# Optimization experiments

Hardware: AMD Instinct MI355X
Metric: run time of the kernel (lower is better)

## Reference

```python
import jax, jax.numpy as jnp
import numpy as np

N = 16384          # number of points (single graph, batch all-zero)
K = 20             # kNN neighbors (DynamicEdgeConv k=20), includes self like torch_cluster.knn
FEATURE_DIM = 128


def setup_inputs() -> dict:
    key = jax.random.key(0)
    ks = jax.random.split(key, 6)
    def lin(k, fan_in, fan_out):
        return (jax.random.normal(k, (fan_in, fan_out), dtype=jnp.float32)
                / np.float32(np.sqrt(fan_in)))
    return {
        "pos": jax.random.normal(ks[0], (N, 3), dtype=jnp.float32),
        "W1": lin(ks[1], 3, 64),    "b1": jnp.zeros((64,), jnp.float32),
        "We1": lin(ks[2], 128, 128), "be1": jnp.zeros((128,), jnp.float32),
        "We2": lin(ks[3], 256, 256), "be2": jnp.zeros((256,), jnp.float32),
        "W2": lin(ks[4], 256, FEATURE_DIM), "b2": jnp.zeros((FEATURE_DIM,), jnp.float32),
    }


def _knn_idx(x, k):
    # kNN graph on current features; indices are non-differentiable (as in PyG).
    x = jax.lax.stop_gradient(x)
    sq = jnp.sum(x * x, axis=-1)                      # [N]
    d2 = sq[:, None] - 2.0 * (x @ x.T) + sq[None, :]  # [N,N] squared distances
    _, idx = jax.lax.top_k(-d2, k)                    # [N,k], self included (d=0)
    return idx


def _edge_conv(x, W, b, k):
    # DynamicEdgeConv: message = MLP([x_i, x_j - x_i]), aggr = max over neighbors
    idx = _knn_idx(x, k)                              # [N,k]
    xj = x[idx]                                       # [N,k,F] gather
    xi = jnp.broadcast_to(x[:, None, :], xj.shape)    # [N,k,F]
    feat = jnp.concatenate([xi, xj - xi], axis=-1)    # [N,k,2F]
    h = jax.nn.relu(feat @ W + b)                     # [N,k,out]
    return jnp.max(h, axis=1)                         # [N,out]


def reference(pos, W1, b1, We1, be1, We2, be2, W2, b2):
    x = jax.nn.relu(pos @ W1 + b1)        # mlp1: 3 -> 64
    x = _edge_conv(x, We1, be1, K)        # lfa1: 2*64 -> 128
    x = _edge_conv(x, We2, be2, K)        # lfa2: 2*128 -> 256
    return x @ W2 + b2                    # mlp2: 256 -> feature_dim
```

## Files before the change

### kernel.cpp

```cpp
#include <hip/hip_runtime.h>
#include <hip/hip_bf16.h>

#define N_PTS 16384
#define KNN   20
#define LIST  32
#define NSPLIT 4

typedef __attribute__((ext_vector_type(8))) short bf16x8;
typedef __attribute__((ext_vector_type(4))) float f32x4;

template<int F>
__device__ __forceinline__ void load_B(const ushort* __restrict__ Xh,
                                       const ushort* __restrict__ Xl,
                                       const float* __restrict__ sqn,
                                       int c0, int ln,
                                       bf16x8 (&bh)[F / 32], bf16x8 (&bl)[F / 32],
                                       float& cn) {
  constexpr int KC = F / 32;
  const int apc = ln >> 4;
  size_t roff = (size_t)(c0 + (ln & 15)) * F;
#pragma unroll
  for (int kc = 0; kc < KC; ++kc) {
    size_t off = roff + (size_t)(kc * 4 + apc) * 8;
    bh[kc] = *(const bf16x8*)(Xh + off);
    bl[kc] = *(const bf16x8*)(Xl + off);
  }
  cn = sqn[c0 + (ln & 15)];
}

template<int F>
__global__ __launch_bounds__(64, 2) void knn_kernel(const ushort* __restrict__ Xh,
                                                    const ushort* __restrict__ Xl,
                                                    const float* __restrict__ sqn,
                                                    int* __restrict__ out_cand) {
  constexpr int KC = F / 32;
  constexpr int NC = N_PTS / NSPLIT;
  constexpr int TS = 16;
  constexpr int NT = NC / TS;
  __shared__ float  Bs[32 * LIST];
  __shared__ ushort Bi[32 * LIST];
  __shared__ float  Ld[32 * LIST];
  __shared__ ushort Li[32 * LIST];

  const int ln = threadIdx.x;
  const int q0 = (int)(blockIdx.x >> 2) * 32;
  const int hf = blockIdx.x & 3;
  const int cbase = hf * NC;

#pragma unroll
  for (int k = 0; k < 16; ++k) {
    int idx = k * 64 + ln;
    Ld[idx] = 3.0e38f; Li[idx] = 0;
  }
  float thr_reg = 3.0e38f;
  float myth[8];
#pragma unroll
  for (int i = 0; i < 8; ++i) myth[i] = 3.0e38f;
  int bcnt = 0;

  auto merge_q = [&](int qk) {
    int cnt = __shfl(bcnt, qk);
    int lrow = qk * LIST;
    float key; int id;
    if (ln < 32) { key = Ld[lrow + ln]; id = (int)Li[lrow + ln]; }
    else {
      int j = ln - 32;
      bool v = j < cnt;
      key = v ? Bs[lrow + j] : 3.0e38f;
      id  = v ? (int)Bi[lrow + j] : 65535;
    }
#pragma unroll
    for (int kk = 2; kk <= 64; kk <<= 1) {
#pragma unroll
      for (int jj = kk >> 1; jj > 0; jj >>= 1) {
        float ok = __shfl_xor(key, jj);
        int   oi = __shfl_xor(id, jj);
        bool pless = (ok < key) || (ok == key && oi < id);
        bool take = pless == (((ln & jj) == 0) == ((ln & kk) == 0));
        key = take ? ok : key;
        id  = take ? oi : id;
      }
    }
    if (ln < 32) { Ld[lrow + ln] = key; Li[lrow + ln] = (ushort)id; }
    float tnew = __shfl(key, 31);
    thr_reg = (ln == qk) ? tnew : thr_reg;
    bcnt    = (ln == qk) ? 0 : bcnt;
  };

  bf16x8 ah[2][KC], al[2][KC];
  {
    const int apc = ln >> 4;
#pragma unroll
    for (int qg = 0; qg < 2; ++qg)
#pragma unroll
      for (int kc = 0; kc < KC; ++kc) {
        size_t off = (size_t)(q0 + qg * 16 + (ln & 15)) * F + (size_t)(kc * 4 + apc) * 8;
        ah[qg][kc] = *(const bf16x8*)(Xh + off);
        al[qg][kc] = *(const bf16x8*)(Xl + off);
      }
  }

  bf16x8 b0h[KC], b0l[KC], b1h[KC], b1l[KC];
  float cn0, cn1;
  load_B<F>(Xh, Xl, sqn, cbase, ln, b0h, b0l, cn0);
  load_B<F>(Xh, Xl, sqn, cbase + TS, ln, b1h, b1l, cn1);

  auto step = [&](bf16x8 (&bh)[KC], bf16x8 (&bl)[KC], float& cn, int t) {
    f32x4 aH[2], aX[2];
#pragma unroll
    for (int qg = 0; qg < 2; ++qg) { aH[qg] = (f32x4){0,0,0,0}; aX[qg] = (f32x4){0,0,0,0}; }
#pragma unroll
    for (int kc = 0; kc < KC; ++kc) {
#pragma unroll
      for (int qg = 0; qg < 2; ++qg) {
        aH[qg] = __builtin_amdgcn_mfma_f32_16x16x32_bf16(ah[qg][kc], bh[kc], aH[qg], 0, 0, 0);
        aX[qg] = __builtin_amdgcn_mfma_f32_16x16x32_bf16(al[qg][kc], bh[kc], aX[qg], 0, 0, 0);
        aX[qg] = __builtin_amdgcn_mfma_f32_16x16x32_bf16(ah[qg][kc], bl[kc], aX[qg], 0, 0, 0);
      }
    }
    float s8[8];
#pragma unroll
    for (int qg = 0; qg < 2; ++qg)
#pragma unroll
      for (int r = 0; r < 4; ++r)
        s8[qg * 4 + r] = cn - 2.0f * (aH[qg][r] + aX[qg][r]);

    if (t + 2 < NT) load_B<F>(Xh, Xl, sqn, cbase + (t + 2) * TS, ln, bh, bl, cn);

    const int ci = cbase + t * TS + (ln & 15);
#pragma unroll
    for (int qg = 0; qg < 2; ++qg)
#pragma unroll
      for (int r = 0; r < 4; ++r) {
        float s = s8[qg * 4 + r];
        unsigned long long m = __ballot(s < myth[qg * 4 + r]);
        if (m) {
          int qk = qg * 16 + ((ln & 48) >> 2) + r;
          int basec = __shfl(bcnt, qk);
          if (s < myth[qg * 4 + r]) {
            int pos = basec +
                __popcll(m & (0xFFFFull << (ln & 48)) & ((1ull << ln) - 1));
            Bs[qk * LIST + pos] = s;
            Bi[qk * LIST + pos] = (ushort)ci;
          }
          if (ln < 32 && (ln >> 4) == qg && (ln & 3) == r)
            bcnt += __popcll((m >> (((ln & 15) >> 2) * 16)) & 0xFFFFull);
        }
      }
    unsigned long long mm = __ballot(ln < 32 && bcnt > 16);
    if (mm) {
      do {
        int qk = __ffsll(mm) - 1;
        mm &= mm - 1;
        merge_q(qk);
      } while (mm);
#pragma unroll
      for (int qg = 0; qg < 2; ++qg)
#pragma unroll
        for (int r = 0; r < 4; ++r)
          myth[qg * 4 + r] = __shfl(thr_reg, qg * 16 + ((ln & 48) >> 2) + r);
    }
  };

#pragma unroll 1
  for (int t = 0; t < NT; t += 2) {
    step(b0h, b0l, cn0, t);
    step(b1h, b1l, cn1, t + 1);
  }

  {
    unsigned long long mm = __ballot(ln < 32 && bcnt > 0);
    while (mm) {
      int qk = __ffsll(mm) - 1;
      mm &= mm - 1;
      merge_q(qk);
    }
  }

#pragma unroll
  for (int k2 = 0; k2 < 16; ++k2) {
    int row = k2 * 2 + (ln >> 5);
    int col = ln & 31;
    out_cand[(size_t)(q0 + row) * (NSPLIT * LIST) + hf * LIST + col] = (int)Li[row * LIST + col];
  }
}

template<int F>
__global__ __launch_bounds__(256) void refine_kernel(const float* __restrict__ X,
                                                     const float* __restrict__ sqn,
                                                     const int* __restrict__ cand,
                                                     int* __restrict__ out_idx) {
  constexpr int CW = NSPLIT * LIST;
  const int wv = threadIdx.x >> 6, ln = threadIdx.x & 63;
  const int q = blockIdx.x * 4 + wv;
  int c0 = cand[(size_t)q * CW + ln];
  int c1 = cand[(size_t)q * CW + 64 + ln];
  const float* qrow = X + (size_t)q * F;
  const float* crow0 = X + (size_t)c0 * F;
  const float* crow1 = X + (size_t)c1 * F;
  float dot0 = 0.f, dot1 = 0.f;
#pragma unroll
  for (int d = 0; d < F; d += 4) {
    float4 qv = *(const float4*)(qrow + d);
    float4 v0 = *(const float4*)(crow0 + d);
    float4 v1 = *(const float4*)(crow1 + d);
    dot0 += qv.x * v0.x + qv.y * v0.y + qv.z * v0.z + qv.w * v0.w;
    dot1 += qv.x * v1.x + qv.y * v1.y + qv.z * v1.z + qv.w * v1.w;
  }
  float s0 = sqn[c0] - 2.0f * dot0;
  float s1 = sqn[c1] - 2.0f * dot1;
  int rank0 = 0, rank1 = 0;
#pragma unroll 1
  for (int j = 0; j < 64; ++j) {
    float a0 = __shfl(s0, j); int i0 = __shfl(c0, j);
    float a1 = __shfl(s1, j); int i1 = __shfl(c1, j);
    rank0 += ((a0 < s0) || (a0 == s0 && i0 < c0)) + ((a1 < s0) || (a1 == s0 && i1 < c0));
    rank1 += ((a0 < s1) || (a0 == s1 && i0 < c1)) + ((a1 < s1) || (a1 == s1 && i1 < c1));
  }
  if (rank0 < KNN) out_idx[(size_t)q * KNN + rank0] = c0;
  if (rank1 < KNN) out_idx[(size_t)q * KNN + rank1] = c1;
}

__global__ __launch_bounds__(256) void mlp1_kernel(const float* __restrict__ pos,
                                                   const float* __restrict__ W1,
                                                   const float* __restrict__ b1,
                                                   float* __restrict__ x1,
                                                   ushort* __restrict__ xh,
                                                   ushort* __restrict__ xl,
                                                   float* __restrict__ sqn) {
  int i = blockIdx.x * 4 + (threadIdx.x >> 6);
  int o = threadIdx.x & 63;
  float p0 = pos[i * 3], p1 = pos[i * 3 + 1], p2 = pos[i * 3 + 2];
  float v = p0 * W1[o] + p1 * W1[64 + o] + p2 * W1[128 + o] + b1[o];
  v = fmaxf(v, 0.f);
  x1[(size_t)i * 64 + o] = v;
  __hip_bfloat16 h = __float2bfloat16(v);
  float hv = __bfloat162float(h);
  __hip_bfloat16 l2 = __float2bfloat16(v - hv);
  xh[(size_t)i * 64 + o] = *(ushort*)&h;
  xl[(size_t)i * 64 + o] = *(ushort*)&l2;
  float ss = v * v;
#pragma unroll
  for (int d = 32; d; d >>= 1) ss += __shfl_xor(ss, d);
  if (o == 0) sqn[i] = ss;
}

template<int F>
__global__ __launch_bounds__(256) void prep_kernel(const float* __restrict__ x,
                                                   ushort* __restrict__ xh,
                                                   ushort* __restrict__ xl,
                                                   float* __restrict__ sqn) {
  int i = blockIdx.x * 4 + (threadIdx.x >> 6);
  int l = threadIdx.x & 63;
  float ss = 0.f;
#pragma unroll
  for (int d = l; d < F; d += 64) {
    float v = x[(size_t)i * F + d];
    ss += v * v;
    __hip_bfloat16 h = __float2bfloat16(v);
    float hv = __bfloat162float(h);
    __hip_bfloat16 l2 = __float2bfloat16(v - hv);
    xh[(size_t)i * F + d] = *(ushort*)&h;
    xl[(size_t)i * F + d] = *(ushort*)&l2;
  }
#pragma unroll
  for (int d = 32; d; d >>= 1) ss += __shfl_xor(ss, d);
  if (l == 0) sqn[i] = ss;
}

template<int K, int OUT, bool BIAS>
__global__ __launch_bounds__(256) void lin_kernel(const float* __restrict__ X,
                                                  const float* __restrict__ W,
                                                  const float* __restrict__ bias,
                                                  float* __restrict__ C) {
  constexpr int XD = OUT / 4;
  constexpr int YD = 256 / XD;
  constexpr int R = YD * 4;
  __shared__ float xs[R * K];
  const int tid = threadIdx.x;
  const int tx = tid % XD, ty = tid / XD;
  const size_t r0 = (size_t)blockIdx.x * R;
  const float4* Xv = (const float4*)(X + r0 * K);
  float4* xsv = (float4*)xs;
#pragma unroll
  for (int i2 = tid; i2 < R * K / 4; i2 += 256) xsv[i2] = Xv[i2];
  __syncthreads();
  float4 acc[4];
#pragma unroll
  for (int i = 0; i < 4; i++) acc[i] = make_float4(0.f, 0.f, 0.f, 0.f);
  const float4* W4 = (const float4*)W;
#pragma unroll 8
  for (int k = 0; k < K; ++k) {
    float4 wv = W4[k * XD + tx];
#pragma unroll
    for (int i = 0; i < 4; i++) {
      float xv = xs[(ty * 4 + i) * K + k];
      acc[i].x += xv * wv.x; acc[i].y += xv * wv.y;
      acc[i].z += xv * wv.z; acc[i].w += xv * wv.w;
    }
  }
  float4 bv = make_float4(0.f, 0.f, 0.f, 0.f);
  if (BIAS) bv = ((const float4*)bias)[tx];
#pragma unroll
  for (int i = 0; i < 4; i++) {
    float4 o;
    o.x = acc[i].x + bv.x; o.y = acc[i].y + bv.y;
    o.z = acc[i].z + bv.z; o.w = acc[i].w + bv.w;
    ((float4*)(C + (r0 + ty * 4 + i) * OUT))[tx] = o;
  }
}

template<int OUT>
__global__ void maxpool_kernel(const float* __restrict__ P, const float* __restrict__ Q,
                               const int* __restrict__ idx, float* __restrict__ xo) {
  __shared__ int nb[KNN];
  int i = blockIdx.x;
  if (threadIdx.x < KNN) nb[threadIdx.x] = idx[(size_t)i * KNN + threadIdx.x];
  __syncthreads();
  int o = threadIdx.x;
  float m = -3.0e38f;
#pragma unroll
  for (int j = 0; j < KNN; j++) m = fmaxf(m, Q[(size_t)nb[j] * OUT + o]);
  float p = P[(size_t)i * OUT + o];
  xo[(size_t)i * OUT + o] = fmaxf(p + m, 0.f);
}

__global__ void wsub_kernel(const float* __restrict__ We, float* __restrict__ Wp, int total) {
  int t = blockIdx.x * 256 + threadIdx.x;
  if (t < total) Wp[t] = We[t] - We[total + t];
}

extern "C" void kernel_launch(void* const* d_in, const int* in_sizes, int n_in,
                              void* d_out, int out_size, void* d_ws, size_t ws_size,
                              hipStream_t stream) {
  const float* pos = (const float*)d_in[0];
  const float* W1  = (const float*)d_in[1];
  const float* b1  = (const float*)d_in[2];
  const float* We1 = (const float*)d_in[3];
  const float* be1 = (const float*)d_in[4];
  const float* We2 = (const float*)d_in[5];
  const float* be2 = (const float*)d_in[6];
  const float* W2  = (const float*)d_in[7];
  const float* b2  = (const float*)d_in[8];
  float* out = (float*)d_out;

  const size_t N = N_PTS;
  float* ws  = (float*)d_ws;
  float* x1  = ws;
  float* P1  = x1 + N * 64;
  float* Q1  = P1 + N * 128;
  float* x2  = Q1 + N * 128;
  float* P2  = x2 + N * 128;
  float* Q2  = P2 + N * 256;
  float* x3  = Q2 + N * 256;
  float* sqn = x3 + N * 256;
  float* Wp1 = sqn + N;
  float* Wp2 = Wp1 + 64 * 128;
  int* idx1  = (int*)(Wp2 + 128 * 256);
  int* idx2  = idx1 + N * KNN;
  int* cand  = (int*)Q2;
  ushort* X1h = (ushort*)(idx2 + N * KNN);
  ushort* X1l = X1h + N * 64;
  ushort* X2h = X1l + N * 64;
  ushort* X2l = X2h + N * 128;
  size_t need = (size_t)((char*)(X2l + N * 128) - (char*)d_ws);
  if (ws_size < need) return;

  wsub_kernel<<<(64 * 128 + 255) / 256, 256, 0, stream>>>(We1, Wp1, 64 * 128);
  wsub_kernel<<<(128 * 256 + 255) / 256, 256, 0, stream>>>(We2, Wp2, 128 * 256);

  mlp1_kernel<<<N / 4, 256, 0, stream>>>(pos, W1, b1, x1, X1h, X1l, sqn);
  knn_kernel<64><<<(N / 32) * NSPLIT, 64, 0, stream>>>(X1h, X1l, sqn, cand);
  refine_kernel<64><<<N / 4, 256, 0, stream>>>(x1, sqn, cand, idx1);
  lin_kernel<64, 128, true ><<<N / 32, 256, 0, stream>>>(x1, Wp1, be1, P1);
  lin_kernel<64, 128, false><<<N / 32, 256, 0, stream>>>(x1, We1 + 64 * 128, nullptr, Q1);
  maxpool_kernel<128><<<N, 128, 0, stream>>>(P1, Q1, idx1, x2);

  prep_kernel<128><<<N / 4, 256, 0, stream>>>(x2, X2h, X2l, sqn);
  knn_kernel<128><<<(N / 32) * NSPLIT, 64, 0, stream>>>(X2h, X2l, sqn, cand);
  refine_kernel<128><<<N / 4, 256, 0, stream>>>(x2, sqn, cand, idx2);
  lin_kernel<128, 256, true ><<<N / 16, 256, 0, stream>>>(x2, Wp2, be2, P2);
  lin_kernel<128, 256, false><<<N / 16, 256, 0, stream>>>(x2, We2 + 128 * 256, nullptr, Q2);
  maxpool_kernel<256><<<N, 256, 0, stream>>>(P2, Q2, idx2, x3);

  lin_kernel<256, 128, true ><<<N / 32, 256, 0, stream>>>(x3, W2, b2, out);
}
```

Baseline: 2.125 ms.

## Split kNN over eight candidate ranges, fuse P/Q linears and maxpool with prep

Doubles the kNN candidate split to 8 chunks, which gives more blocks and a higher occupancy hint. Per-lane bucket counters replace shuffles in the insertion path, and the MFMA section is wrapped in s_setprio. The refine kernel now ranks 256 candidates per query. The two P/Q linear layers are fused into one kernel that reads X once, and the first maxpool is fused with the bf16 hi/lo split and norm computation, removing a kernel launch and a pass over x2. The trade-off is more candidates to refine and more output traffic for the candidate lists.

```diff
diff --git a/kernel.cpp b/kernel.cpp
--- a/kernel.cpp
+++ b/kernel.cpp
@@ -4,7 +4,7 @@
 #define N_PTS 16384
 #define KNN   20
 #define LIST  32
-#define NSPLIT 4
+#define NSPLIT 8
 
 typedef __attribute__((ext_vector_type(8))) short bf16x8;
 typedef __attribute__((ext_vector_type(4))) float f32x4;
@@ -29,7 +29,7 @@
 }
 
 template<int F>
-__global__ __launch_bounds__(64, 2) void knn_kernel(const ushort* __restrict__ Xh,
+__global__ __launch_bounds__(64, 4) void knn_kernel(const ushort* __restrict__ Xh,
                                                     const ushort* __restrict__ Xl,
                                                     const float* __restrict__ sqn,
                                                     int* __restrict__ out_cand) {
@@ -43,8 +43,8 @@
   __shared__ ushort Li[32 * LIST];
 
   const int ln = threadIdx.x;
-  const int q0 = (int)(blockIdx.x >> 2) * 32;
-  const int hf = blockIdx.x & 3;
+  const int q0 = (int)(blockIdx.x >> 3) * 32;
+  const int hf = blockIdx.x & 7;
   const int cbase = hf * NC;
 
 #pragma unroll
@@ -54,8 +54,9 @@
   }
   float thr_reg = 3.0e38f;
   float myth[8];
-#pragma unroll
-  for (int i = 0; i < 8; ++i) myth[i] = 3.0e38f;
+  int   cnt8[8];
+#pragma unroll
+  for (int i = 0; i < 8; ++i) { myth[i] = 3.0e38f; cnt8[i] = 0; }
   int bcnt = 0;
 
   auto merge_q = [&](int qk) {
@@ -85,6 +86,11 @@
     float tnew = __shfl(key, 31);
     thr_reg = (ln == qk) ? tnew : thr_reg;
     bcnt    = (ln == qk) ? 0 : bcnt;
+    int slot = (qk >> 2) & 3;
+    int g = ((qk >> 4) << 2) + (qk & 3);
+#pragma unroll
+    for (int i = 0; i < 8; ++i)
+      if (i == g && (ln >> 4) == slot) cnt8[i] = 0;
   };
 
   bf16x8 ah[2][KC], al[2][KC];
@@ -105,10 +111,14 @@
   load_B<F>(Xh, Xl, sqn, cbase, ln, b0h, b0l, cn0);
   load_B<F>(Xh, Xl, sqn, cbase + TS, ln, b1h, b1l, cn1);
 
+  const unsigned long long gmask = 0xFFFFull << (ln & 48);
+  const unsigned long long below = (1ull << ln) - 1;
+
   auto step = [&](bf16x8 (&bh)[KC], bf16x8 (&bl)[KC], float& cn, int t) {
     f32x4 aH[2], aX[2];
 #pragma unroll
     for (int qg = 0; qg < 2; ++qg) { aH[qg] = (f32x4){0,0,0,0}; aX[qg] = (f32x4){0,0,0,0}; }
+    __builtin_amdgcn_s_setprio(1);
 #pragma unroll
     for (int kc = 0; kc < KC; ++kc) {
 #pragma unroll
@@ -118,6 +128,7 @@
         aX[qg] = __builtin_amdgcn_mfma_f32_16x16x32_bf16(ah[qg][kc], bl[kc], aX[qg], 0, 0, 0);
       }
     }
+    __builtin_amdgcn_s_setprio(0);
     float s8[8];
 #pragma unroll
     for (int qg = 0; qg < 2; ++qg)
@@ -132,17 +143,17 @@
     for (int qg = 0; qg < 2; ++qg)
 #pragma unroll
       for (int r = 0; r < 4; ++r) {
-        float s = s8[qg * 4 + r];
-        unsigned long long m = __ballot(s < myth[qg * 4 + r]);
+        const int g = qg * 4 + r;
+        float s = s8[g];
+        unsigned long long m = __ballot(s < myth[g]);
         if (m) {
-          int qk = qg * 16 + ((ln & 48) >> 2) + r;
-          int basec = __shfl(bcnt, qk);
-          if (s < myth[qg * 4 + r]) {
-            int pos = basec +
-                __popcll(m & (0xFFFFull << (ln & 48)) & ((1ull << ln) - 1));
+          if (s < myth[g]) {
+            int qk = qg * 16 + ((ln & 48) >> 2) + r;
+            int pos = cnt8[g] + __popcll(m & gmask & below);
             Bs[qk * LIST + pos] = s;
             Bi[qk * LIST + pos] = (ushort)ci;
           }
+          cnt8[g] += __popcll(m & gmask);
           if (ln < 32 && (ln >> 4) == qg && (ln & 3) == r)
             bcnt += __popcll((m >> (((ln & 15) >> 2) * 16)) & 0xFFFFull);
         }
@@ -193,32 +204,37 @@
   constexpr int CW = NSPLIT * LIST;
   const int wv = threadIdx.x >> 6, ln = threadIdx.x & 63;
   const int q = blockIdx.x * 4 + wv;
-  int c0 = cand[(size_t)q * CW + ln];
-  int c1 = cand[(size_t)q * CW + 64 + ln];
+  int c[4]; float s[4];
+#pragma unroll
+  for (int i = 0; i < 4; ++i) c[i] = cand[(size_t)q * CW + i * 64 + ln];
   const float* qrow = X + (size_t)q * F;
-  const float* crow0 = X + (size_t)c0 * F;
-  const float* crow1 = X + (size_t)c1 * F;
-  float dot0 = 0.f, dot1 = 0.f;
-#pragma unroll
-  for (int d = 0; d < F; d += 4) {
-    float4 qv = *(const float4*)(qrow + d);
-    float4 v0 = *(const float4*)(crow0 + d);
-    float4 v1 = *(const float4*)(crow1 + d);
-    dot0 += qv.x * v0.x + qv.y * v0.y + qv.z * v0.z + qv.w * v0.w;
-    dot1 += qv.x * v1.x + qv.y * v1.y + qv.z * v1.z + qv.w * v1.w;
-  }
-  float s0 = sqn[c0] - 2.0f * dot0;
-  float s1 = sqn[c1] - 2.0f * dot1;
-  int rank0 = 0, rank1 = 0;
+#pragma unroll
+  for (int i = 0; i < 4; ++i) {
+    const float* crow = X + (size_t)c[i] * F;
+    float dot = 0.f;
+#pragma unroll
+    for (int d = 0; d < F; d += 4) {
+      float4 qv = *(const float4*)(qrow + d);
+      float4 cv = *(const float4*)(crow + d);
+      dot += qv.x * cv.x + qv.y * cv.y + qv.z * cv.z + qv.w * cv.w;
+    }
+    s[i] = sqn[c[i]] - 2.0f * dot;
+  }
+  int rank[4] = {0, 0, 0, 0};
 #pragma unroll 1
   for (int j = 0; j < 64; ++j) {
-    float a0 = __shfl(s0, j); int i0 = __shfl(c0, j);
-    float a1 = __shfl(s1, j); int i1 = __shfl(c1, j);
-    rank0 += ((a0 < s0) || (a0 == s0 && i0 < c0)) + ((a1 < s0) || (a1 == s0 && i1 < c0));
-    rank1 += ((a0 < s1) || (a0 == s1 && i0 < c1)) + ((a1 < s1) || (a1 == s1 && i1 < c1));
-  }
-  if (rank0 < KNN) out_idx[(size_t)q * KNN + rank0] = c0;
-  if (rank1 < KNN) out_idx[(size_t)q * KNN + rank1] = c1;
+#pragma unroll
+    for (int a = 0; a < 4; ++a) {
+      float sa = __shfl(s[a], j);
+      int   ca = __shfl(c[a], j);
+#pragma unroll
+      for (int b = 0; b < 4; ++b)
+        rank[b] += (sa < s[b]) || (sa == s[b] && ca < c[b]);
+    }
+  }
+#pragma unroll
+  for (int i = 0; i < 4; ++i)
+    if (rank[i] < KNN) out_idx[(size_t)q * KNN + rank[i]] = c[i];
 }
 
 __global__ __launch_bounds__(256) void mlp1_kernel(const float* __restrict__ pos,
@@ -245,27 +261,92 @@
   if (o == 0) sqn[i] = ss;
 }
 
-template<int F>
-__global__ __launch_bounds__(256) void prep_kernel(const float* __restrict__ x,
-                                                   ushort* __restrict__ xh,
-                                                   ushort* __restrict__ xl,
-                                                   float* __restrict__ sqn) {
-  int i = blockIdx.x * 4 + (threadIdx.x >> 6);
-  int l = threadIdx.x & 63;
-  float ss = 0.f;
-#pragma unroll
-  for (int d = l; d < F; d += 64) {
-    float v = x[(size_t)i * F + d];
-    ss += v * v;
-    __hip_bfloat16 h = __float2bfloat16(v);
-    float hv = __bfloat162float(h);
-    __hip_bfloat16 l2 = __float2bfloat16(v - hv);
-    xh[(size_t)i * F + d] = *(ushort*)&h;
-    xl[(size_t)i * F + d] = *(ushort*)&l2;
-  }
+template<int K, int OUT>
+__global__ __launch_bounds__(256) void linpq_kernel(const float* __restrict__ X,
+                                                    const float* __restrict__ Wp,
+                                                    const float* __restrict__ bp,
+                                                    const float* __restrict__ Wq,
+                                                    float* __restrict__ P,
+                                                    float* __restrict__ Q) {
+  constexpr int XD = OUT / 4;
+  constexpr int YD = 256 / XD;
+  constexpr int R = YD * 4;
+  __shared__ float xs[R * K];
+  const int tid = threadIdx.x;
+  const int tx = tid % XD, ty = tid / XD;
+  const size_t r0 = (size_t)blockIdx.x * R;
+  const float4* Xv = (const float4*)(X + r0 * K);
+  float4* xsv = (float4*)xs;
+#pragma unroll
+  for (int i2 = tid; i2 < R * K / 4; i2 += 256) xsv[i2] = Xv[i2];
+  __syncthreads();
+  float4 ap[4], aq[4];
+#pragma unroll
+  for (int i = 0; i < 4; i++) { ap[i] = make_float4(0,0,0,0); aq[i] = make_float4(0,0,0,0); }
+  const float4* Wp4 = (const float4*)Wp;
+  const float4* Wq4 = (const float4*)Wq;
+#pragma unroll 4
+  for (int k = 0; k < K; ++k) {
+    float4 wp = Wp4[k * XD + tx];
+    float4 wq = Wq4[k * XD + tx];
+#pragma unroll
+    for (int i = 0; i < 4; i++) {
+      float xv = xs[(ty * 4 + i) * K + k];
+      ap[i].x += xv * wp.x; ap[i].y += xv * wp.y; ap[i].z += xv * wp.z; ap[i].w += xv * wp.w;
+      aq[i].x += xv * wq.x; aq[i].y += xv * wq.y; aq[i].z += xv * wq.z; aq[i].w += xv * wq.w;
+    }
+  }
+  float4 bv = ((const float4*)bp)[tx];
+#pragma unroll
+  for (int i = 0; i < 4; i++) {
+    float4 o;
+    o.x = ap[i].x + bv.x; o.y = ap[i].y + bv.y; o.z = ap[i].z + bv.z; o.w = ap[i].w + bv.w;
+    ((float4*)(P + (r0 + ty * 4 + i) * OUT))[tx] = o;
+    ((float4*)(Q + (r0 + ty * 4 + i) * OUT))[tx] = aq[i];
+  }
+}
+
+__global__ void maxpoolprep_kernel(const float* __restrict__ P, const float* __restrict__ Qm,
+                                   const int* __restrict__ idx, float* __restrict__ xo,
+                                   ushort* __restrict__ xh, ushort* __restrict__ xl,
+                                   float* __restrict__ sqn) {
+  __shared__ int nb[KNN];
+  __shared__ float part[2];
+  int i = blockIdx.x;
+  if (threadIdx.x < KNN) nb[threadIdx.x] = idx[(size_t)i * KNN + threadIdx.x];
+  __syncthreads();
+  int o = threadIdx.x;
+  float m = -3.0e38f;
+#pragma unroll
+  for (int j = 0; j < KNN; j++) m = fmaxf(m, Qm[(size_t)nb[j] * 128 + o]);
+  float v = fmaxf(P[(size_t)i * 128 + o] + m, 0.f);
+  xo[(size_t)i * 128 + o] = v;
+  __hip_bfloat16 h = __float2bfloat16(v);
+  float hv = __bfloat162float(h);
+  __hip_bfloat16 l2 = __float2bfloat16(v - hv);
+  xh[(size_t)i * 128 + o] = *(ushort*)&h;
+  xl[(size_t)i * 128 + o] = *(ushort*)&l2;
+  float ss = v * v;
 #pragma unroll
   for (int d = 32; d; d >>= 1) ss += __shfl_xor(ss, d);
-  if (l == 0) sqn[i] = ss;
+  if ((threadIdx.x & 63) == 0) part[threadIdx.x >> 6] = ss;
+  __syncthreads();
+  if (threadIdx.x == 0) sqn[i] = part[0] + part[1];
+}
+
+template<int OUT>
+__global__ void maxpool_kernel(const float* __restrict__ P, const float* __restrict__ Q,
+                               const int* __restrict__ idx, float* __restrict__ xo) {
+  __shared__ int nb[KNN];
+  int i = blockIdx.x;
+  if (threadIdx.x < KNN) nb[threadIdx.x] = idx[(size_t)i * KNN + threadIdx.x];
+  __syncthreads();
+  int o = threadIdx.x;
+  float m = -3.0e38f;
+#pragma unroll
+  for (int j = 0; j < KNN; j++) m = fmaxf(m, Q[(size_t)nb[j] * OUT + o]);
+  float p = P[(size_t)i * OUT + o];
+  xo[(size_t)i * OUT + o] = fmaxf(p + m, 0.f);
 }
 
 template<int K, int OUT, bool BIAS>
@@ -308,21 +389,6 @@
     o.z = acc[i].z + bv.z; o.w = acc[i].w + bv.w;
     ((float4*)(C + (r0 + ty * 4 + i) * OUT))[tx] = o;
   }
-}
-
-template<int OUT>
-__global__ void maxpool_kernel(const float* __restrict__ P, const float* __restrict__ Q,
-                               const int* __restrict__ idx, float* __restrict__ xo) {
-  __shared__ int nb[KNN];
-  int i = blockIdx.x;
-  if (threadIdx.x < KNN) nb[threadIdx.x] = idx[(size_t)i * KNN + threadIdx.x];
-  __syncthreads();
-  int o = threadIdx.x;
-  float m = -3.0e38f;
-#pragma unroll
-  for (int j = 0; j < KNN; j++) m = fmaxf(m, Q[(size_t)nb[j] * OUT + o]);
-  float p = P[(size_t)i * OUT + o];
-  xo[(size_t)i * OUT + o] = fmaxf(p + m, 0.f);
 }
 
 __global__ void wsub_kernel(const float* __restrict__ We, float* __restrict__ Wp, int total) {
@@ -372,15 +438,12 @@
   mlp1_kernel<<<N / 4, 256, 0, stream>>>(pos, W1, b1, x1, X1h, X1l, sqn);
   knn_kernel<64><<<(N / 32) * NSPLIT, 64, 0, stream>>>(X1h, X1l, sqn, cand);
   refine_kernel<64><<<N / 4, 256, 0, stream>>>(x1, sqn, cand, idx1);
-  lin_kernel<64, 128, true ><<<N / 32, 256, 0, stream>>>(x1, Wp1, be1, P1);
-  lin_kernel<64, 128, false><<<N / 32, 256, 0, stream>>>(x1, We1 + 64 * 128, nullptr, Q1);
-  maxpool_kernel<128><<<N, 128, 0, stream>>>(P1, Q1, idx1, x2);
-
-  prep_kernel<128><<<N / 4, 256, 0, stream>>>(x2, X2h, X2l, sqn);
+  linpq_kernel<64, 128><<<N / 32, 256, 0, stream>>>(x1, Wp1, be1, We1 + 64 * 128, P1, Q1);
+  maxpoolprep_kernel<<<N, 128, 0, stream>>>(P1, Q1, idx1, x2, X2h, X2l, sqn);
+
   knn_kernel<128><<<(N / 32) * NSPLIT, 64, 0, stream>>>(X2h, X2l, sqn, cand);
   refine_kernel<128><<<N / 4, 256, 0, stream>>>(x2, sqn, cand, idx2);
-  lin_kernel<128, 256, true ><<<N / 16, 256, 0, stream>>>(x2, Wp2, be2, P2);
-  lin_kernel<128, 256, false><<<N / 16, 256, 0, stream>>>(x2, We2 + 128 * 256, nullptr, Q2);
+  linpq_kernel<128, 256><<<N / 16, 256, 0, stream>>>(x2, Wp2, be2, We2 + 128 * 256, P2, Q2);
   maxpool_kernel<256><<<N, 256, 0, stream>>>(P2, Q2, idx2, x3);
 
   lin_kernel<256, 128, true ><<<N / 32, 256, 0, stream>>>(x3, W2, b2, out);
```

Result: slower. 4.788 ms (median of 2 runs) (+125.4%).
